# Kernel tuning notes

Measured on AMD Instinct MI355X. Metric: run time of the kernel, lower is better.

Reference implementation:

```python
import jax, jax.numpy as jnp
import numpy as np

D = 768          # n_embd
I = 3072         # moe_intermediate_size (4 * n_embd)
E = 8            # n_routed_experts
K = 2            # num_experts_per_tok
LIMIT = 10.0     # swiglu_limit
VOCAB = 32768


def setup_inputs() -> dict:
    key = jax.random.key(0)
    ks = jax.random.split(key, 10)
    s = 0.02
    return {
        "x": jax.random.normal(ks[0], (1, 2048, D), dtype=jnp.float32),
        "input_ids": jax.random.randint(ks[1], (1, 2048), 0, VOCAB, dtype=jnp.int64),
        "gate_w": jax.random.normal(ks[2], (D, E), dtype=jnp.float32) * s,
        "gate_bias": jnp.zeros((E,), dtype=jnp.float32),
        "w1": jax.random.normal(ks[3], (E, D, I), dtype=jnp.float32) * s,
        "w2": jax.random.normal(ks[4], (E, I, D), dtype=jnp.float32) * s,
        "w3": jax.random.normal(ks[5], (E, D, I), dtype=jnp.float32) * s,
        "w1s": jax.random.normal(ks[6], (D, I), dtype=jnp.float32) * s,
        "w2s": jax.random.normal(ks[7], (I, D), dtype=jnp.float32) * s,
        "w3s": jax.random.normal(ks[8], (D, I), dtype=jnp.float32) * s,
    }


def _expert(xf, W1, W2, W3):
    # SwiGLU with asymmetric clamping, as in DeepSeekExpert (swiglu_limit > 0)
    gate = jnp.minimum(xf @ W1, LIMIT)               # clamp max only
    up = jnp.clip(xf @ W3, -LIMIT, LIMIT)            # clamp both sides
    return (jax.nn.silu(gate) * up) @ W2


def reference(x, input_ids, gate_w, gate_bias, w1, w2, w3, w1s, w2s, w3s):
    B, T, _ = x.shape
    flat = x.reshape(-1, D)                           # [N, D], N = B*T
    N = flat.shape[0]

    # gating: sqrtsoftplus scoring
    scores = jnp.sqrt(jax.nn.softplus(flat @ gate_w))  # [N, E]
    routed_scores = scores + gate_bias                 # gate_bias used only for topk selection
    _, indices = jax.lax.top_k(routed_scores, K)       # [N, K]

    weights = jnp.take_along_axis(scores, indices, axis=1)  # [N, K]
    # norm_topk_prob=True; routed_scaling_factor=1.0
    weights = weights / jnp.clip(weights.sum(axis=-1, keepdims=True), 1e-6)

    # dense combine matrix [N, E] (jit-friendly dispatch/combine)
    combine = jnp.zeros((N, E), dtype=weights.dtype)
    combine = combine.at[jnp.arange(N)[:, None], indices].add(weights)

    # shared expert on all tokens
    y = _expert(flat, w1s, w2s, w3s)                   # [N, D]

    # routed experts: batched grouped GEMM over all tokens, then weighted combine
    gate_h = jnp.minimum(jnp.einsum('td,edi->eti', flat, w1), LIMIT)   # [E, N, I]
    up_h = jnp.clip(jnp.einsum('td,edi->eti', flat, w3), -LIMIT, LIMIT)
    h = jax.nn.silu(gate_h) * up_h                     # [E, N, I]
    out_e = jnp.einsum('eti,eid->etd', h, w2)          # [E, N, D]
    routed = jnp.einsum('etd,te->td', out_e, combine)  # [N, D]

    return (y + routed).reshape(B, T, D)
```

## Files before the change

kernel.cpp:

```cpp
#include <hip/hip_runtime.h>


#define D_ 768
#define I_ 3072
#define E_ 8
#define NTOK 2048
#define NPMAX 5120
#define MAXTILES 40
#define NSHT 16
#define ROWS (NTOK + NPMAX)
#define SPLITK 2
#define KS_ (I_ / SPLITK)

typedef __bf16 bf16x8 __attribute__((ext_vector_type(8)));
typedef float floatx4 __attribute__((ext_vector_type(4)));

#define GLOAD_LDS16(g, l) __builtin_amdgcn_global_load_lds( \
    (const __attribute__((address_space(1))) void*)(g),     \
    (__attribute__((address_space(3))) void*)(l), 16, 0, 0)

__device__ __forceinline__ unsigned short f2b(float f) {
    unsigned int u = __float_as_uint(f);
    u += 0x7fffu + ((u >> 16) & 1u);
    return (unsigned short)(u >> 16);
}

__device__ __forceinline__ void transpose_tile(const float* __restrict__ s,
                                               unsigned short* __restrict__ d,
                                               int R, int C, int r0, int c0,
                                               float (*t)[65], int tid) {
#pragma unroll
    for (int j = 0; j < 4; j++) {
        int slot = tid + j * 256;
        int rr = slot >> 4, c4 = (slot & 15) * 4;
        float4 v = *(const float4*)(s + (size_t)(r0 + rr) * C + c0 + c4);
        t[rr][c4] = v.x; t[rr][c4 + 1] = v.y; t[rr][c4 + 2] = v.z; t[rr][c4 + 3] = v.w;
    }
    __syncthreads();
#pragma unroll
    for (int j = 0; j < 2; j++) {
        int slot = tid + j * 256;
        int c = slot >> 3, rs = (slot & 7) * 8;
        unsigned short o[8] __attribute__((aligned(16)));
#pragma unroll
        for (int i = 0; i < 8; i++) o[i] = f2b(t[rs + i][c]);
        *(int4*)(d + (size_t)(c0 + c) * R + r0 + rs) = *(const int4*)o;
    }
}


__global__ __launch_bounds__(256) void prep_lite_kernel(
    const float* __restrict__ x, const float* __restrict__ gw,
    const float* __restrict__ gbias,
    const float* __restrict__ w1s, const float* __restrict__ w3s,
    const float* __restrict__ w2s,
    unsigned short* __restrict__ xb,
    unsigned short* __restrict__ w1sb, unsigned short* __restrict__ w3sb,
    unsigned short* __restrict__ w2sb,
    int* __restrict__ idx, float* __restrict__ wts) {
    __shared__ float t[64][65];
    int b = blockIdx.x, tid = threadIdx.x;
    if (b < 1728) {
        int z = b / 576, r = b % 576;
        if (z < 2) {
            int bx = r % 48, by = r / 48;
            transpose_tile(z ? w3s : w1s, z ? w3sb : w1sb, D_, I_,
                           by * 64, bx * 64, t, tid);
        } else {
            int tx = r % 12, ty = r / 12;
            transpose_tile(w2s, w2sb, I_, D_, ty * 64, tx * 64, t, tid);
        }
    } else if (b < 3264) {
        int gid = (b - 1728) * 256 + tid;
        float4 v = *(const float4*)(x + (size_t)gid * 4);
        ushort4 o;
        o.x = f2b(v.x); o.y = f2b(v.y); o.z = f2b(v.z); o.w = f2b(v.w);
        *(ushort4*)(xb + (size_t)gid * 4) = o;
    } else {
        int tok = (b - 3264) * 4 + (tid >> 6);
        int lane = tid & 63;
        float z[E_];
#pragma unroll
        for (int e = 0; e < E_; e++) z[e] = 0.f;
        const float* xr = x + (size_t)tok * D_;
        for (int j = lane; j < D_; j += 64) {
            float xv = xr[j];
            const float* g = gw + (size_t)j * E_;
#pragma unroll
            for (int e = 0; e < E_; e++) z[e] += xv * g[e];
        }
#pragma unroll
        for (int off = 32; off > 0; off >>= 1)
#pragma unroll
            for (int e = 0; e < E_; e++) z[e] += __shfl_down(z[e], off, 64);
        if (lane == 0) {
            float s[E_], r[E_];
#pragma unroll
            for (int e = 0; e < E_; e++) {
                float zz = z[e];
                float sp = zz > 0.f ? zz + log1pf(expf(-zz)) : log1pf(expf(zz));
                s[e] = sqrtf(sp);
                r[e] = s[e] + gbias[e];
            }
            int i0 = 0;
            for (int e = 1; e < E_; e++) if (r[e] > r[i0]) i0 = e;
            int i1 = (i0 == 0) ? 1 : 0;
            for (int e = 0; e < E_; e++) if (e != i0 && r[e] > r[i1]) i1 = e;
            float w0 = s[i0], w1v = s[i1];
            float inv = 1.f / fmaxf(w0 + w1v, 1e-6f);
            idx[2 * tok] = i0; idx[2 * tok + 1] = i1;
            wts[2 * tok] = w0 * inv; wts[2 * tok + 1] = w1v * inv;
        }
    }
}


__launch_bounds__(256)
__global__ void gemm_shared_kernel(const unsigned short* __restrict__ xb,
                                   const unsigned short* __restrict__ w1sb,
                                   const unsigned short* __restrict__ w3sb,
                                   unsigned short* __restrict__ act,
                                   const float* __restrict__ w1,
                                   const float* __restrict__ w3,
                                   unsigned short* __restrict__ w1b,
                                   unsigned short* __restrict__ w3b,
                                   const int* __restrict__ idx,
                                   const float* __restrict__ wts,
                                   int* __restrict__ pair_token,
                                   float* __restrict__ pair_w,
                                   int* __restrict__ pos_of,
                                   int* __restrict__ tiles) {
    __shared__ __align__(16) unsigned short smem[128 * 64 + 64 * 64 + 64 * 64];
    unsigned short* As  = smem;
    unsigned short* Bs1 = smem + 128 * 64;
    unsigned short* Bs3 = smem + 128 * 64 + 64 * 64;

    int bxi = blockIdx.x, byi = blockIdx.y, tid = threadIdx.x;

    if (byi == 0) {
        if (bxi) return;
        int* cnt = (int*)smem; int* seg = cnt + E_; int* cur = cnt + 2 * E_;
        if (tid < E_) { cnt[tid] = 0; cur[tid] = 0; }
        __syncthreads();
        for (int p = tid; p < NTOK * 2; p += 256) atomicAdd(&cnt[idx[p]], 1);
        __syncthreads();
        if (tid == 0) {
            int off = 0, nt = 0;
            for (int e = 0; e < E_; e++) {
                seg[e] = off;
                int te = (cnt[e] + 127) >> 7;
                for (int j = 0; j < te; j++) {
                    tiles[nt * 2] = e; tiles[nt * 2 + 1] = off + j * 128; nt++;
                }
                off += te * 128;
            }
            for (; nt < MAXTILES; nt++) { tiles[nt * 2] = -1; tiles[nt * 2 + 1] = 0; }
        }
        for (int p = tid; p < NPMAX; p += 256) pair_token[p] = -1;
        __syncthreads();
        for (int p = tid; p < NTOK * 2; p += 256) {
            int e = idx[p];
            int r = atomicAdd(&cur[e], 1);
            int pos = seg[e] + r;
            pair_token[pos] = p >> 1;
            pair_w[pos] = wts[p];
            pos_of[p] = pos;
        }
        return;
    }

    int t = byi - 1;
    if (t % 13) {
        int slot = t - t / 13 - 1;
        int b2 = slot * 48 + bxi;
        int z = b2 / 576, r = b2 % 576;
        int bx = r % 48, by = r / 48;
        const float* s; unsigned short* d;
        if (z < 8) { s = w1 + (size_t)z * D_ * I_;       d = w1b + (size_t)z * D_ * I_; }
        else       { s = w3 + (size_t)(z - 8) * D_ * I_; d = w3b + (size_t)(z - 8) * D_ * I_; }
        transpose_tile(s, d, D_, I_, by * 64, bx * 64, (float(*)[65])smem, tid);
        return;
    }

    int mt = t / 13;
    int m0 = mt * 128;
    int n0 = bxi * 64;
    int lane = tid & 63, wave = tid >> 6;
    int wm = (wave & 1) * 64, wn = (wave >> 1) * 32;
    int l15 = lane & 15, quad = lane >> 4;

    int rl = lane >> 3, ph = lane & 7, lg = ph ^ rl;
    const unsigned short* asrc[4];
#pragma unroll
    for (int j = 0; j < 4; j++)
        asrc[j] = xb + (size_t)(m0 + j * 32 + wave * 8 + rl) * D_ + lg * 8;
    const unsigned short *b1src[2], *b3src[2];
#pragma unroll
    for (int j = 0; j < 2; j++) {
        int r = j * 32 + wave * 8 + rl;
        b1src[j] = w1sb + (size_t)(n0 + r) * D_ + lg * 8;
        b3src[j] = w3sb + (size_t)(n0 + r) * D_ + lg * 8;
    }
    unsigned short *ldA[4], *ldB1[2], *ldB3[2];
#pragma unroll
    for (int j = 0; j < 4; j++) ldA[j] = As + (j * 32 + wave * 8) * 64;
#pragma unroll
    for (int j = 0; j < 2; j++) {
        ldB1[j] = Bs1 + (j * 32 + wave * 8) * 64;
        ldB3[j] = Bs3 + (j * 32 + wave * 8) * 64;
    }

    floatx4 acc1[4][2] = {}; floatx4 acc3[4][2] = {};
    int sx = (l15 & 7);

    for (int k0 = 0; k0 < D_; k0 += 64) {
        __syncthreads();
#pragma unroll
        for (int j = 0; j < 4; j++) GLOAD_LDS16(asrc[j] + k0, ldA[j]);
#pragma unroll
        for (int j = 0; j < 2; j++) {
            GLOAD_LDS16(b1src[j] + k0, ldB1[j]);
            GLOAD_LDS16(b3src[j] + k0, ldB3[j]);
        }
        __syncthreads();

#pragma unroll
        for (int kk = 0; kk < 2; kk++) {
            int pq = ((kk * 4 + quad) ^ sx) * 8;
            bf16x8 af[4], b1f[2], b3f[2];
#pragma unroll
            for (int mi = 0; mi < 4; mi++)
                af[mi] = *(const bf16x8*)(As + (wm + mi * 16 + l15) * 64 + pq);
#pragma unroll
            for (int ni = 0; ni < 2; ni++) {
                b1f[ni] = *(const bf16x8*)(Bs1 + (wn + ni * 16 + l15) * 64 + pq);
                b3f[ni] = *(const bf16x8*)(Bs3 + (wn + ni * 16 + l15) * 64 + pq);
            }
#pragma unroll
            for (int mi = 0; mi < 4; mi++)
#pragma unroll
                for (int ni = 0; ni < 2; ni++) {
                    acc1[mi][ni] = __builtin_amdgcn_mfma_f32_16x16x32_bf16(
                        af[mi], b1f[ni], acc1[mi][ni], 0, 0, 0);
                    acc3[mi][ni] = __builtin_amdgcn_mfma_f32_16x16x32_bf16(
                        af[mi], b3f[ni], acc3[mi][ni], 0, 0, 0);
                }
        }
    }

#pragma unroll
    for (int mi = 0; mi < 4; mi++)
#pragma unroll
        for (int ni = 0; ni < 2; ni++) {
            int col = n0 + wn + ni * 16 + l15;
#pragma unroll
            for (int rr = 0; rr < 4; rr++) {
                int row = m0 + wm + mi * 16 + quad * 4 + rr;
                float g = fminf(acc1[mi][ni][rr], 10.f);
                float u = fminf(fmaxf(acc3[mi][ni][rr], -10.f), 10.f);
                float a = g / (1.f + __expf(-g)) * u;
                act[(size_t)row * I_ + col] = f2b(a);
            }
        }
}


__launch_bounds__(256)
__global__ void gemm_routed_kernel(const unsigned short* __restrict__ xb,
                                   const unsigned short* __restrict__ w1b,
                                   const unsigned short* __restrict__ w3b,
                                   const int* __restrict__ tiles,
                                   const int* __restrict__ pair_token,
                                   unsigned short* __restrict__ act,
                                   const float* __restrict__ w2,
                                   unsigned short* __restrict__ w2b) {
    __shared__ __align__(16) unsigned short smem[128 * 64 + 64 * 64 + 64 * 64];
    unsigned short* As  = smem;
    unsigned short* Bs1 = smem + 128 * 64;
    unsigned short* Bs3 = smem + 128 * 64 + 64 * 64;

    int bxi = blockIdx.x, byi = blockIdx.y, tid = threadIdx.x;
    int g = byi / 17, h = byi % 17;

    if (h >= 5) {
        int slot = g * 12 + (h - 5);
        int b2 = slot * 48 + bxi;
        int z = b2 / 576, r = b2 % 576;
        int tx = r % 12, ty = r / 12;
        transpose_tile(w2 + (size_t)z * I_ * D_, w2b + (size_t)z * I_ * D_,
                       I_, D_, ty * 64, tx * 64, (float(*)[65])smem, tid);
        return;
    }

    int mt = g * 5 + h;
    int e = tiles[mt * 2];
    if (e < 0) return;
    int m0 = NTOK + tiles[mt * 2 + 1];
    const unsigned short* B1 = w1b + (size_t)e * I_ * D_;
    const unsigned short* B3 = w3b + (size_t)e * I_ * D_;

    int n0 = bxi * 64;
    int lane = tid & 63, wave = tid >> 6;
    int wm = (wave & 1) * 64, wn = (wave >> 1) * 32;
    int l15 = lane & 15, quad = lane >> 4;

    int rl = lane >> 3, ph = lane & 7, lg = ph ^ rl;
    const unsigned short* asrc[4];
#pragma unroll
    for (int j = 0; j < 4; j++) {
        int r = j * 32 + wave * 8 + rl;
        int tok = pair_token[m0 - NTOK + r]; if (tok < 0) tok = 0;
        asrc[j] = xb + (size_t)tok * D_ + lg * 8;
    }
    const unsigned short *b1src[2], *b3src[2];
#pragma unroll
    for (int j = 0; j < 2; j++) {
        int r = j * 32 + wave * 8 + rl;
        b1src[j] = B1 + (size_t)(n0 + r) * D_ + lg * 8;
        b3src[j] = B3 + (size_t)(n0 + r) * D_ + lg * 8;
    }
    unsigned short *ldA[4], *ldB1[2], *ldB3[2];
#pragma unroll
    for (int j = 0; j < 4; j++) ldA[j] = As + (j * 32 + wave * 8) * 64;
#pragma unroll
    for (int j = 0; j < 2; j++) {
        ldB1[j] = Bs1 + (j * 32 + wave * 8) * 64;
        ldB3[j] = Bs3 + (j * 32 + wave * 8) * 64;
    }

    floatx4 acc1[4][2] = {}; floatx4 acc3[4][2] = {};
    int sx = (l15 & 7);

    for (int k0 = 0; k0 < D_; k0 += 64) {
        __syncthreads();
#pragma unroll
        for (int j = 0; j < 4; j++) GLOAD_LDS16(asrc[j] + k0, ldA[j]);
#pragma unroll
        for (int j = 0; j < 2; j++) {
            GLOAD_LDS16(b1src[j] + k0, ldB1[j]);
            GLOAD_LDS16(b3src[j] + k0, ldB3[j]);
        }
        __syncthreads();

#pragma unroll
        for (int kk = 0; kk < 2; kk++) {
            int pq = ((kk * 4 + quad) ^ sx) * 8;
            bf16x8 af[4], b1f[2], b3f[2];
#pragma unroll
            for (int mi = 0; mi < 4; mi++)
                af[mi] = *(const bf16x8*)(As + (wm + mi * 16 + l15) * 64 + pq);
#pragma unroll
            for (int ni = 0; ni < 2; ni++) {
                b1f[ni] = *(const bf16x8*)(Bs1 + (wn + ni * 16 + l15) * 64 + pq);
                b3f[ni] = *(const bf16x8*)(Bs3 + (wn + ni * 16 + l15) * 64 + pq);
            }
#pragma unroll
            for (int mi = 0; mi < 4; mi++)
#pragma unroll
                for (int ni = 0; ni < 2; ni++) {
                    acc1[mi][ni] = __builtin_amdgcn_mfma_f32_16x16x32_bf16(
                        af[mi], b1f[ni], acc1[mi][ni], 0, 0, 0);
                    acc3[mi][ni] = __builtin_amdgcn_mfma_f32_16x16x32_bf16(
                        af[mi], b3f[ni], acc3[mi][ni], 0, 0, 0);
                }
        }
    }

#pragma unroll
    for (int mi = 0; mi < 4; mi++)
#pragma unroll
        for (int ni = 0; ni < 2; ni++) {
            int col = n0 + wn + ni * 16 + l15;
#pragma unroll
            for (int rr = 0; rr < 4; rr++) {
                int row = m0 + wm + mi * 16 + quad * 4 + rr;
                float g = fminf(acc1[mi][ni][rr], 10.f);
                float u = fminf(fmaxf(acc3[mi][ni][rr], -10.f), 10.f);
                float a = g / (1.f + __expf(-g)) * u;
                act[(size_t)row * I_ + col] = f2b(a);
            }
        }
}


__launch_bounds__(256)
__global__ void gemm_out_kernel(const unsigned short* __restrict__ act,
                                const unsigned short* __restrict__ w2sb,
                                const unsigned short* __restrict__ w2b,
                                const int* __restrict__ tiles,
                                float* __restrict__ outp) {
    __shared__ __align__(16) unsigned short As[128 * 64];
    __shared__ __align__(16) unsigned short Bs[64 * 64];

    int mt = blockIdx.y, ks = blockIdx.z;
    int kbase = ks * KS_;
    const unsigned short* B;
    int m0;
    if (mt < NSHT) {
        B = w2sb; m0 = mt * 128;
    } else {
        int e = tiles[(mt - NSHT) * 2];
        if (e < 0) return;
        m0 = NTOK + tiles[(mt - NSHT) * 2 + 1];
        B = w2b + (size_t)e * I_ * D_;
    }
    float* C = outp + (size_t)ks * ROWS * D_;
    int n0 = blockIdx.x * 64;
    int tid = threadIdx.x;
    int lane = tid & 63, wave = tid >> 6;
    int wm = (wave & 1) * 64, wn = (wave >> 1) * 32;
    int l15 = lane & 15, quad = lane >> 4;

    int rl = lane >> 3, ph = lane & 7, lg = ph ^ rl;
    const unsigned short* asrc[4];
#pragma unroll
    for (int j = 0; j < 4; j++)
        asrc[j] = act + (size_t)(m0 + j * 32 + wave * 8 + rl) * I_ + kbase + lg * 8;
    const unsigned short* bsrc[2];
#pragma unroll
    for (int j = 0; j < 2; j++)
        bsrc[j] = B + (size_t)(n0 + j * 32 + wave * 8 + rl) * I_ + kbase + lg * 8;
    unsigned short *ldA[4], *ldB[2];
#pragma unroll
    for (int j = 0; j < 4; j++) ldA[j] = As + (j * 32 + wave * 8) * 64;
#pragma unroll
    for (int j = 0; j < 2; j++) ldB[j] = Bs + (j * 32 + wave * 8) * 64;

    floatx4 acc[4][2] = {};
    int sx = (l15 & 7);

    for (int k0 = 0; k0 < KS_; k0 += 64) {
        __syncthreads();
#pragma unroll
        for (int j = 0; j < 4; j++) GLOAD_LDS16(asrc[j] + k0, ldA[j]);
#pragma unroll
        for (int j = 0; j < 2; j++) GLOAD_LDS16(bsrc[j] + k0, ldB[j]);
        __syncthreads();

#pragma unroll
        for (int kk = 0; kk < 2; kk++) {
            int pq = ((kk * 4 + quad) ^ sx) * 8;
            bf16x8 af[4], bf[2];
#pragma unroll
            for (int mi = 0; mi < 4; mi++)
                af[mi] = *(const bf16x8*)(As + (wm + mi * 16 + l15) * 64 + pq);
#pragma unroll
            for (int ni = 0; ni < 2; ni++)
                bf[ni] = *(const bf16x8*)(Bs + (wn + ni * 16 + l15) * 64 + pq);
#pragma unroll
            for (int mi = 0; mi < 4; mi++)
#pragma unroll
                for (int ni = 0; ni < 2; ni++)
                    acc[mi][ni] = __builtin_amdgcn_mfma_f32_16x16x32_bf16(
                        af[mi], bf[ni], acc[mi][ni], 0, 0, 0);
        }
    }

#pragma unroll
    for (int mi = 0; mi < 4; mi++)
#pragma unroll
        for (int ni = 0; ni < 2; ni++) {
            int col = n0 + wn + ni * 16 + l15;
#pragma unroll
            for (int rr = 0; rr < 4; rr++) {
                int row = m0 + wm + mi * 16 + quad * 4 + rr;
                C[(size_t)row * D_ + col] = acc[mi][ni][rr];
            }
        }
}


__global__ void combine_kernel(const float* __restrict__ outp,
                               const int* __restrict__ pos_of,
                               const float* __restrict__ pair_w,
                               float* __restrict__ out) {
    int gid = blockIdx.x * 256 + threadIdx.x;
    int t = gid / (D_ / 4);
    int j = (gid % (D_ / 4)) * 4;
    int p0 = pos_of[2 * t], p1 = pos_of[2 * t + 1];
    float w0 = pair_w[p0], w1 = pair_w[p1];
    float a0 = 0.f, a1 = 0.f, a2 = 0.f, a3 = 0.f;
#pragma unroll
    for (int ks = 0; ks < SPLITK; ks++) {
        const float* P = outp + (size_t)ks * ROWS * D_;
        float4 a = *(const float4*)(P + (size_t)t * D_ + j);
        float4 b = *(const float4*)(P + (size_t)(NTOK + p0) * D_ + j);
        float4 c = *(const float4*)(P + (size_t)(NTOK + p1) * D_ + j);
        a0 += a.x + w0 * b.x + w1 * c.x;
        a1 += a.y + w0 * b.y + w1 * c.y;
        a2 += a.z + w0 * b.z + w1 * c.z;
        a3 += a.w + w0 * b.w + w1 * c.w;
    }
    float4 o; o.x = a0; o.y = a1; o.z = a2; o.w = a3;
    *(float4*)(out + (size_t)t * D_ + j) = o;
}


extern "C" void kernel_launch(void* const* d_in, const int* in_sizes, int n_in,
                              void* d_out, int out_size, void* d_ws, size_t ws_size,
                              hipStream_t stream) {
    (void)in_sizes; (void)n_in; (void)out_size; (void)ws_size;
    const float* x   = (const float*)d_in[0];
    const float* gw  = (const float*)d_in[2];
    const float* gb  = (const float*)d_in[3];
    const float* w1  = (const float*)d_in[4];
    const float* w2  = (const float*)d_in[5];
    const float* w3  = (const float*)d_in[6];
    const float* w1s = (const float*)d_in[7];
    const float* w2s = (const float*)d_in[8];
    const float* w3s = (const float*)d_in[9];
    float* out = (float*)d_out;

    char* ws = (char*)d_ws;
    size_t off = 0;
    auto alloc = [&](size_t bytes) {
        size_t o = (off + 255) & ~(size_t)255;
        off = o + bytes;
        return (void*)(ws + o);
    };
    unsigned short* xb   = (unsigned short*)alloc((size_t)NTOK * D_ * 2);
    unsigned short* w1b  = (unsigned short*)alloc((size_t)E_ * I_ * D_ * 2);
    unsigned short* w3b  = (unsigned short*)alloc((size_t)E_ * I_ * D_ * 2);
    unsigned short* w2b  = (unsigned short*)alloc((size_t)E_ * I_ * D_ * 2);
    unsigned short* w1sb = (unsigned short*)alloc((size_t)I_ * D_ * 2);
    unsigned short* w3sb = (unsigned short*)alloc((size_t)I_ * D_ * 2);
    unsigned short* w2sb = (unsigned short*)alloc((size_t)I_ * D_ * 2);
    unsigned short* act  = (unsigned short*)alloc((size_t)ROWS * I_ * 2);
    float* outp = (float*)alloc((size_t)SPLITK * ROWS * D_ * 4);
    int*   idx  = (int*)alloc((size_t)NTOK * 2 * 4);
    float* wts  = (float*)alloc((size_t)NTOK * 2 * 4);
    int*   ptok = (int*)alloc((size_t)NPMAX * 4);
    float* pw   = (float*)alloc((size_t)NPMAX * 4);
    int*   posf = (int*)alloc((size_t)NTOK * 2 * 4);
    int*   tls  = (int*)alloc((size_t)MAXTILES * 2 * 4);

    prep_lite_kernel<<<3776, 256, 0, stream>>>(x, gw, gb, w1s, w3s, w2s,
                                               xb, w1sb, w3sb, w2sb, idx, wts);
    gemm_shared_kernel<<<dim3(48, 209), 256, 0, stream>>>(
        xb, w1sb, w3sb, act, w1, w3, w1b, w3b, idx, wts, ptok, pw, posf, tls);
    gemm_routed_kernel<<<dim3(48, 136), 256, 0, stream>>>(
        xb, w1b, w3b, tls, ptok, act, w2, w2b);
    gemm_out_kernel<<<dim3(D_ / 64, NSHT + MAXTILES, SPLITK), 256, 0, stream>>>(
        act, w2sb, w2b, tls, outp);
    combine_kernel<<<NTOK * (D_ / 4) / 256, 256, 0, stream>>>(outp, posf, pw, out);
}
```

Baseline: 436.9 us.

## Use 128-row bf16 transpose tiles and move shared down-proj into routed kernel

The weight transpose now converts to bf16 before staging in LDS and uses 128x64 tiles with a swizzled layout. This halves the number of transpose blocks and LDS traffic per element. The shared expert's down-projection GEMM, now full-K with no split, moves out of gemm_out_kernel and into extra blocks of gemm_routed_kernel, so it overlaps with the routed up-projection and w2 transposes. The combine kernel is adjusted because shared rows now live only in the first partial buffer. Grid interleave ratios are re-tuned to match.

Result: slower. 457.0 us (+4.6%).

```diff
diff --git a/kernel.cpp b/kernel.cpp
--- a/kernel.cpp
+++ b/kernel.cpp
@@ -25,26 +25,30 @@
     return (unsigned short)(u >> 16);
 }
 
-__device__ __forceinline__ void transpose_tile(const float* __restrict__ s,
-                                               unsigned short* __restrict__ d,
-                                               int R, int C, int r0, int c0,
-                                               float (*t)[65], int tid) {
+__device__ __forceinline__ void transpose_tile128(
+    const float* __restrict__ s, unsigned short* __restrict__ d,
+    int R, int C, int r0, int c0, unsigned short* t, int tid) {
+#pragma unroll
+    for (int j = 0; j < 8; j++) {
+        int slot = tid + j * 256;
+        int rr = slot >> 4;
+        int gr = slot & 15;
+        float4 v = *(const float4*)(s + (size_t)(r0 + rr) * C + c0 + gr * 4);
+        unsigned short o[4] __attribute__((aligned(8)));
+        o[0] = f2b(v.x); o[1] = f2b(v.y); o[2] = f2b(v.z); o[3] = f2b(v.w);
+        *(uint2*)(t + rr * 64 + 4 * ((gr + (rr >> 3)) & 15)) = *(const uint2*)o;
+    }
+    __syncthreads();
 #pragma unroll
     for (int j = 0; j < 4; j++) {
         int slot = tid + j * 256;
-        int rr = slot >> 4, c4 = (slot & 15) * 4;
-        float4 v = *(const float4*)(s + (size_t)(r0 + rr) * C + c0 + c4);
-        t[rr][c4] = v.x; t[rr][c4 + 1] = v.y; t[rr][c4 + 2] = v.z; t[rr][c4 + 3] = v.w;
-    }
-    __syncthreads();
-#pragma unroll
-    for (int j = 0; j < 2; j++) {
-        int slot = tid + j * 256;
-        int c = slot >> 3, rs = (slot & 7) * 8;
+        int c = slot >> 4;
+        int m = slot & 15;
+        int base = (c & 3) + 4 * (((c >> 2) + m) & 15);
         unsigned short o[8] __attribute__((aligned(16)));
 #pragma unroll
-        for (int i = 0; i < 8; i++) o[i] = f2b(t[rs + i][c]);
-        *(int4*)(d + (size_t)(c0 + c) * R + r0 + rs) = *(const int4*)o;
+        for (int i = 0; i < 8; i++) o[i] = t[(m * 8 + i) * 64 + base];
+        *(int4*)(d + (size_t)(c0 + c) * R + r0 + m * 8) = *(const int4*)o;
     }
 }
 
@@ -58,26 +62,26 @@
     unsigned short* __restrict__ w1sb, unsigned short* __restrict__ w3sb,
     unsigned short* __restrict__ w2sb,
     int* __restrict__ idx, float* __restrict__ wts) {
-    __shared__ float t[64][65];
+    __shared__ unsigned short t[128 * 64];
     int b = blockIdx.x, tid = threadIdx.x;
-    if (b < 1728) {
-        int z = b / 576, r = b % 576;
+    if (b < 864) {
+        int z = b / 288, r = b % 288;
         if (z < 2) {
-            int bx = r % 48, by = r / 48;
-            transpose_tile(z ? w3s : w1s, z ? w3sb : w1sb, D_, I_,
-                           by * 64, bx * 64, t, tid);
+            int by = r / 48, bx = r % 48;
+            transpose_tile128(z ? w3s : w1s, z ? w3sb : w1sb, D_, I_,
+                              by * 128, bx * 64, t, tid);
         } else {
-            int tx = r % 12, ty = r / 12;
-            transpose_tile(w2s, w2sb, I_, D_, ty * 64, tx * 64, t, tid);
-        }
-    } else if (b < 3264) {
-        int gid = (b - 1728) * 256 + tid;
+            int by = r / 12, bx = r % 12;
+            transpose_tile128(w2s, w2sb, I_, D_, by * 128, bx * 64, t, tid);
+        }
+    } else if (b < 2400) {
+        int gid = (b - 864) * 256 + tid;
         float4 v = *(const float4*)(x + (size_t)gid * 4);
         ushort4 o;
         o.x = f2b(v.x); o.y = f2b(v.y); o.z = f2b(v.z); o.w = f2b(v.w);
         *(ushort4*)(xb + (size_t)gid * 4) = o;
     } else {
-        int tok = (b - 3264) * 4 + (tid >> 6);
+        int tok = (b - 2400) * 4 + (tid >> 6);
         int lane = tid & 63;
         float z[E_];
 #pragma unroll
@@ -170,19 +174,19 @@
     }
 
     int t = byi - 1;
-    if (t % 13) {
-        int slot = t - t / 13 - 1;
+    if (t % 7) {
+        int slot = t - t / 7 - 1;
         int b2 = slot * 48 + bxi;
-        int z = b2 / 576, r = b2 % 576;
-        int bx = r % 48, by = r / 48;
+        int z = b2 / 288, r = b2 % 288;
+        int by = r / 48, bx = r % 48;
         const float* s; unsigned short* d;
         if (z < 8) { s = w1 + (size_t)z * D_ * I_;       d = w1b + (size_t)z * D_ * I_; }
         else       { s = w3 + (size_t)(z - 8) * D_ * I_; d = w3b + (size_t)(z - 8) * D_ * I_; }
-        transpose_tile(s, d, D_, I_, by * 64, bx * 64, (float(*)[65])smem, tid);
+        transpose_tile128(s, d, D_, I_, by * 128, bx * 64, smem, tid);
         return;
     }
 
-    int mt = t / 13;
+    int mt = t / 7;
     int m0 = mt * 128;
     int n0 = bxi * 64;
     int lane = tid & 63, wave = tid >> 6;
@@ -273,38 +277,98 @@
                                    const int* __restrict__ pair_token,
                                    unsigned short* __restrict__ act,
                                    const float* __restrict__ w2,
-                                   unsigned short* __restrict__ w2b) {
+                                   unsigned short* __restrict__ w2b,
+                                   const unsigned short* __restrict__ w2sb,
+                                   float* __restrict__ outp) {
     __shared__ __align__(16) unsigned short smem[128 * 64 + 64 * 64 + 64 * 64];
     unsigned short* As  = smem;
     unsigned short* Bs1 = smem + 128 * 64;
     unsigned short* Bs3 = smem + 128 * 64 + 64 * 64;
 
     int bxi = blockIdx.x, byi = blockIdx.y, tid = threadIdx.x;
-    int g = byi / 17, h = byi % 17;
-
-    if (h >= 5) {
-        int slot = g * 12 + (h - 5);
+    int g = byi / 23, h = byi % 23;
+    int lane = tid & 63, wave = tid >> 6;
+    int wm = (wave & 1) * 64, wn = (wave >> 1) * 32;
+    int l15 = lane & 15, quad = lane >> 4;
+    int rl = lane >> 3, ph = lane & 7, lg = ph ^ rl;
+    int sx = (l15 & 7);
+
+    if (h == 22) {
+        int id2 = g * 48 + bxi;
+        int mt2 = id2 / 12, nx = id2 % 12;
+        int m0 = mt2 * 128, n0 = nx * 64;
+        const unsigned short* asrc[4];
+#pragma unroll
+        for (int j = 0; j < 4; j++)
+            asrc[j] = act + (size_t)(m0 + j * 32 + wave * 8 + rl) * I_ + lg * 8;
+        const unsigned short* bsrc[2];
+#pragma unroll
+        for (int j = 0; j < 2; j++)
+            bsrc[j] = w2sb + (size_t)(n0 + j * 32 + wave * 8 + rl) * I_ + lg * 8;
+        unsigned short *ldA[4], *ldB[2];
+#pragma unroll
+        for (int j = 0; j < 4; j++) ldA[j] = As + (j * 32 + wave * 8) * 64;
+#pragma unroll
+        for (int j = 0; j < 2; j++) ldB[j] = Bs1 + (j * 32 + wave * 8) * 64;
+
+        floatx4 acc[4][2] = {};
+        for (int k0 = 0; k0 < I_; k0 += 64) {
+            __syncthreads();
+#pragma unroll
+            for (int j = 0; j < 4; j++) GLOAD_LDS16(asrc[j] + k0, ldA[j]);
+#pragma unroll
+            for (int j = 0; j < 2; j++) GLOAD_LDS16(bsrc[j] + k0, ldB[j]);
+            __syncthreads();
+#pragma unroll
+            for (int kk = 0; kk < 2; kk++) {
+                int pq = ((kk * 4 + quad) ^ sx) * 8;
+                bf16x8 af[4], bf[2];
+#pragma unroll
+                for (int mi = 0; mi < 4; mi++)
+                    af[mi] = *(const bf16x8*)(As + (wm + mi * 16 + l15) * 64 + pq);
+#pragma unroll
+                for (int ni = 0; ni < 2; ni++)
+                    bf[ni] = *(const bf16x8*)(Bs1 + (wn + ni * 16 + l15) * 64 + pq);
+#pragma unroll
+                for (int mi = 0; mi < 4; mi++)
+#pragma unroll
+                    for (int ni = 0; ni < 2; ni++)
+                        acc[mi][ni] = __builtin_amdgcn_mfma_f32_16x16x32_bf16(
+                            af[mi], bf[ni], acc[mi][ni], 0, 0, 0);
+            }
+        }
+#pragma unroll
+        for (int mi = 0; mi < 4; mi++)
+#pragma unroll
+            for (int ni = 0; ni < 2; ni++) {
+                int col = n0 + wn + ni * 16 + l15;
+#pragma unroll
+                for (int rr = 0; rr < 4; rr++) {
+                    int row = m0 + wm + mi * 16 + quad * 4 + rr;
+                    outp[(size_t)row * D_ + col] = acc[mi][ni][rr];
+                }
+            }
+        return;
+    }
+
+    if (h >= 10) {
+        int slot = g * 12 + (h - 10);
         int b2 = slot * 48 + bxi;
-        int z = b2 / 576, r = b2 % 576;
-        int tx = r % 12, ty = r / 12;
-        transpose_tile(w2 + (size_t)z * I_ * D_, w2b + (size_t)z * I_ * D_,
-                       I_, D_, ty * 64, tx * 64, (float(*)[65])smem, tid);
+        int z = b2 / 288, r = b2 % 288;
+        int by = r / 12, bx = r % 12;
+        transpose_tile128(w2 + (size_t)z * I_ * D_, w2b + (size_t)z * I_ * D_,
+                          I_, D_, by * 128, bx * 64, smem, tid);
         return;
     }
 
-    int mt = g * 5 + h;
+    int mt = g * 10 + h;
     int e = tiles[mt * 2];
     if (e < 0) return;
     int m0 = NTOK + tiles[mt * 2 + 1];
     const unsigned short* B1 = w1b + (size_t)e * I_ * D_;
     const unsigned short* B3 = w3b + (size_t)e * I_ * D_;
-
     int n0 = bxi * 64;
-    int lane = tid & 63, wave = tid >> 6;
-    int wm = (wave & 1) * 64, wn = (wave >> 1) * 32;
-    int l15 = lane & 15, quad = lane >> 4;
-
-    int rl = lane >> 3, ph = lane & 7, lg = ph ^ rl;
+
     const unsigned short* asrc[4];
 #pragma unroll
     for (int j = 0; j < 4; j++) {
@@ -329,7 +393,6 @@
     }
 
     floatx4 acc1[4][2] = {}; floatx4 acc3[4][2] = {};
-    int sx = (l15 & 7);
 
     for (int k0 = 0; k0 < D_; k0 += 64) {
         __syncthreads();
@@ -374,9 +437,9 @@
 #pragma unroll
             for (int rr = 0; rr < 4; rr++) {
                 int row = m0 + wm + mi * 16 + quad * 4 + rr;
-                float g = fminf(acc1[mi][ni][rr], 10.f);
+                float gg = fminf(acc1[mi][ni][rr], 10.f);
                 float u = fminf(fmaxf(acc3[mi][ni][rr], -10.f), 10.f);
-                float a = g / (1.f + __expf(-g)) * u;
+                float a = gg / (1.f + __expf(-gg)) * u;
                 act[(size_t)row * I_ + col] = f2b(a);
             }
         }
@@ -385,7 +448,6 @@
 
 __launch_bounds__(256)
 __global__ void gemm_out_kernel(const unsigned short* __restrict__ act,
-                                const unsigned short* __restrict__ w2sb,
                                 const unsigned short* __restrict__ w2b,
                                 const int* __restrict__ tiles,
                                 float* __restrict__ outp) {
@@ -394,16 +456,10 @@
 
     int mt = blockIdx.y, ks = blockIdx.z;
     int kbase = ks * KS_;
-    const unsigned short* B;
-    int m0;
-    if (mt < NSHT) {
-        B = w2sb; m0 = mt * 128;
-    } else {
-        int e = tiles[(mt - NSHT) * 2];
-        if (e < 0) return;
-        m0 = NTOK + tiles[(mt - NSHT) * 2 + 1];
-        B = w2b + (size_t)e * I_ * D_;
-    }
+    int e = tiles[mt * 2];
+    if (e < 0) return;
+    int m0 = NTOK + tiles[mt * 2 + 1];
+    const unsigned short* B = w2b + (size_t)e * I_ * D_;
     float* C = outp + (size_t)ks * ROWS * D_;
     int n0 = blockIdx.x * 64;
     int tid = threadIdx.x;
@@ -479,19 +535,18 @@
     int j = (gid % (D_ / 4)) * 4;
     int p0 = pos_of[2 * t], p1 = pos_of[2 * t + 1];
     float w0 = pair_w[p0], w1 = pair_w[p1];
-    float a0 = 0.f, a1 = 0.f, a2 = 0.f, a3 = 0.f;
-#pragma unroll
-    for (int ks = 0; ks < SPLITK; ks++) {
-        const float* P = outp + (size_t)ks * ROWS * D_;
-        float4 a = *(const float4*)(P + (size_t)t * D_ + j);
-        float4 b = *(const float4*)(P + (size_t)(NTOK + p0) * D_ + j);
-        float4 c = *(const float4*)(P + (size_t)(NTOK + p1) * D_ + j);
-        a0 += a.x + w0 * b.x + w1 * c.x;
-        a1 += a.y + w0 * b.y + w1 * c.y;
-        a2 += a.z + w0 * b.z + w1 * c.z;
-        a3 += a.w + w0 * b.w + w1 * c.w;
-    }
-    float4 o; o.x = a0; o.y = a1; o.z = a2; o.w = a3;
+    const float* P0 = outp;
+    const float* P1 = outp + (size_t)ROWS * D_;
+    float4 a  = *(const float4*)(P0 + (size_t)t * D_ + j);
+    float4 b0 = *(const float4*)(P0 + (size_t)(NTOK + p0) * D_ + j);
+    float4 b1 = *(const float4*)(P1 + (size_t)(NTOK + p0) * D_ + j);
+    float4 c0 = *(const float4*)(P0 + (size_t)(NTOK + p1) * D_ + j);
+    float4 c1 = *(const float4*)(P1 + (size_t)(NTOK + p1) * D_ + j);
+    float4 o;
+    o.x = a.x + w0 * (b0.x + b1.x) + w1 * (c0.x + c1.x);
+    o.y = a.y + w0 * (b0.y + b1.y) + w1 * (c0.y + c1.y);
+    o.z = a.z + w0 * (b0.z + b1.z) + w1 * (c0.z + c1.z);
+    o.w = a.w + w0 * (b0.w + b1.w) + w1 * (c0.w + c1.w);
     *(float4*)(out + (size_t)t * D_ + j) = o;
 }
 
@@ -534,13 +589,13 @@
     int*   posf = (int*)alloc((size_t)NTOK * 2 * 4);
     int*   tls  = (int*)alloc((size_t)MAXTILES * 2 * 4);
 
-    prep_lite_kernel<<<3776, 256, 0, stream>>>(x, gw, gb, w1s, w3s, w2s,
+    prep_lite_kernel<<<2912, 256, 0, stream>>>(x, gw, gb, w1s, w3s, w2s,
                                                xb, w1sb, w3sb, w2sb, idx, wts);
-    gemm_shared_kernel<<<dim3(48, 209), 256, 0, stream>>>(
+    gemm_shared_kernel<<<dim3(48, 113), 256, 0, stream>>>(
         xb, w1sb, w3sb, act, w1, w3, w1b, w3b, idx, wts, ptok, pw, posf, tls);
-    gemm_routed_kernel<<<dim3(48, 136), 256, 0, stream>>>(
-        xb, w1b, w3b, tls, ptok, act, w2, w2b);
-    gemm_out_kernel<<<dim3(D_ / 64, NSHT + MAXTILES, SPLITK), 256, 0, stream>>>(
-        act, w2sb, w2b, tls, outp);
+    gemm_routed_kernel<<<dim3(48, 92), 256, 0, stream>>>(
+        xb, w1b, w3b, tls, ptok, act, w2, w2b, w2sb, outp);
+    gemm_out_kernel<<<dim3(D_ / 64, MAXTILES, SPLITK), 256, 0, stream>>>(
+        act, w2b, tls, outp);
     combine_kernel<<<NTOK * (D_ / 4) / 256, 256, 0, stream>>>(outp, posf, pw, out);
 }
```
